# Kernel optimization log

Measured on AMD Instinct MI355X. Metric: run time of the kernel, lower is better.

Reference implementation:

```python
import jax, jax.numpy as jnp
import numpy as np


def binarize(x):
    # sign to +/-1 (>=0 -> 1); forward value only (STE handled in bwd module)
    return jnp.where(x >= 0, 1.0, -1.0).astype(x.dtype)


def setup_inputs() -> dict:
    key = jax.random.key(0)
    k1, k2, k3 = jax.random.split(key, 3)
    B, D_IN, D_H, D_OUT = 16384, 4096, 4096, 1
    x = jax.random.normal(k1, (B, D_IN), dtype=jnp.float32)
    W1 = jax.random.normal(k2, (D_H, D_IN), dtype=jnp.float32) * 0.02
    W2 = jax.random.normal(k3, (D_OUT, D_H), dtype=jnp.float32) * 0.02
    return {"x": x, "W1": W1, "W2": W2}


def reference(x, W1, W2):
    # fc1: BinaryLinear (binarized weight, no bias) + BinaryTanh (hardtanh then sign)
    h = x @ binarize(W1).T                      # [B, D_H]
    h = binarize(jnp.clip(h, -1.0, 1.0))        # hardtanh + binarize -> +/-1
    # fc2: BinaryLinear + Sigmoid
    out = jax.nn.sigmoid(h @ binarize(W2).T)    # [B, 1]
    y_hat = jnp.squeeze((out >= 0.5).astype(jnp.float32))  # [B]
    return out, y_hat
```

## Files before the change

kernel.cpp:

```cpp
#include <hip/hip_runtime.h>
#include <stdint.h>


typedef int v4i  __attribute__((ext_vector_type(4)));
typedef int v16i __attribute__((ext_vector_type(16)));

#define B_ROWS   16384
#define DIM      4096
#define MT       64
#define NT       128
#define KT       64

#define WS_LOGIT  0
#define WS_W2S    65536
#define WS_B      69632
#define WS_A      (69632 + 16777216)
#define WS_NEEDED ((size_t)WS_A + 268435456ULL)

__device__ __forceinline__ void dma16(const void* g, void* l) {
    __builtin_amdgcn_global_load_lds(
        (const __attribute__((address_space(1))) void*)g,
        (__attribute__((address_space(3))) void*)l, 16, 0, 0);
}

__global__ void pack_x_frag_kernel(const float* __restrict__ x, int8_t* __restrict__ wsA) {
    __shared__ __align__(16) int8_t tile[16384];
    const int mb32 = blockIdx.x, t = threadIdx.x;
    const int r = t >> 3;
    const int c = t & 7;
    const int kh = (c >> 2) & 1;
    const int L = kh * 32 + r;
    const int ldsQ = L * 16 + (c & 3) * 4;
    const float* srcRow = x + ((size_t)(mb32 * 32 + r) << 12);
    int8_t* dstBase = wsA + ((size_t)mb32 << 19);

    for (int kw = 0; kw < 32; ++kw) {
#pragma unroll
        for (int i = 0; i < 4; ++i) {
            const int j = c + 8 * i;
            float4 f = ((const float4*)(srcRow + (kw << 7)))[j];
            float fv[4] = {f.x, f.y, f.z, f.w};
            int dig[4][4];
#pragma unroll
            for (int e = 0; e < 4; ++e) {
                int v = __float2int_rn(fv[e] * 67108864.0f);
#pragma unroll
                for (int d = 0; d < 4; ++d) {
                    int b = (int)(int8_t)(v & 0xff);
                    dig[e][d] = b & 0xff;
                    v = (v - b) >> 8;
                }
            }
#pragma unroll
            for (int d = 0; d < 4; ++d) {
                uint32_t wrd = (uint32_t)dig[0][d] | ((uint32_t)dig[1][d] << 8)
                             | ((uint32_t)dig[2][d] << 16) | ((uint32_t)dig[3][d] << 24);
                *(uint32_t*)(tile + i * 4096 + d * 1024 + ldsQ) = wrd;
            }
        }
        __syncthreads();
        {
            const int4* s = (const int4*)tile;
            int4* dst = (int4*)(dstBase + ((size_t)kw << 14));
#pragma unroll
            for (int q = 0; q < 4; ++q) dst[t + 256 * q] = s[t + 256 * q];
        }
        __syncthreads();
    }
}

__global__ void pack_x_kernel(float* __restrict__ x) {
    const int b = blockIdx.x, t = threadIdx.x;
    float* row = x + (size_t)b * DIM;
    float f[16];
#pragma unroll
    for (int i = 0; i < 4; ++i) {
        float4 v = ((const float4*)(row + t * 16))[i];
        f[i*4+0] = v.x; f[i*4+1] = v.y; f[i*4+2] = v.z; f[i*4+3] = v.w;
    }
    __syncthreads();
    uint32_t wds[4][4];
#pragma unroll
    for (int j = 0; j < 4; ++j) {
#pragma unroll
        for (int d = 0; d < 4; ++d) wds[d][j] = 0u;
#pragma unroll
        for (int i = 0; i < 4; ++i) {
            int v = __float2int_rn(f[j*4+i] * 67108864.0f);
#pragma unroll
            for (int d = 0; d < 4; ++d) {
                int bb = (int)(int8_t)(v & 0xff);
                wds[d][j] |= (uint32_t)(bb & 0xff) << (8 * i);
                v = (v - bb) >> 8;
            }
        }
    }
    int8_t* rowb = (int8_t*)row;
#pragma unroll
    for (int d = 0; d < 4; ++d) {
        int4 o; o.x = (int)wds[d][0]; o.y = (int)wds[d][1];
        o.z = (int)wds[d][2]; o.w = (int)wds[d][3];
        *(int4*)(rowb + d * DIM + t * 16) = o;
    }
}

__global__ void pack_w1_kernel(const float* __restrict__ W1, int8_t* __restrict__ wsB) {
    const int tg = blockIdx.x * 256 + threadIdx.x;
    const int n  = tg >> 8;
    const int k0 = (tg & 255) << 4;
    const float* src = W1 + (size_t)n * DIM + k0;
    uint32_t w[4];
#pragma unroll
    for (int j = 0; j < 4; ++j) {
        float4 v = ((const float4*)src)[j];
        uint32_t b0 = (v.x >= 0.f) ? 0x01u : 0xFFu;
        uint32_t b1 = (v.y >= 0.f) ? 0x01u : 0xFFu;
        uint32_t b2 = (v.z >= 0.f) ? 0x01u : 0xFFu;
        uint32_t b3 = (v.w >= 0.f) ? 0x01u : 0xFFu;
        w[j] = b0 | (b1 << 8) | (b2 << 16) | (b3 << 24);
    }
    const int nb = n >> 7, kt = k0 >> 6;
    const int nsub = (n >> 5) & 3, ks = (k0 >> 5) & 1;
    const int L = (n & 31) | (((k0 >> 4) & 1) << 5);
    const size_t off = ((size_t)(nb * 64 + kt) << 13) + (nsub << 11) + (ks << 10) + (L << 4);
    int4 o; o.x = (int)w[0]; o.y = (int)w[1]; o.z = (int)w[2]; o.w = (int)w[3];
    *(int4*)(wsB + off) = o;
}

__global__ void pack_w2_kernel(const float* __restrict__ W2, int8_t* __restrict__ w2s) {
    const int j = blockIdx.x * 256 + threadIdx.x;
    if (j < DIM) w2s[j] = (W2[j] >= 0.f) ? (int8_t)1 : (int8_t)-1;
}

#define LOAD_AF(dst, kt_) do {                                             \
    const int8_t* _p = aBase + ((size_t)(kt_) << 13);                      \
    _Pragma("unroll") for (int _s = 0; _s < 2; ++_s)                       \
    _Pragma("unroll") for (int _d = 0; _d < 4; ++_d)                       \
        dst[_s * 4 + _d] = *(const v4i*)(_p + (_s << 12) + (_d << 10));    \
} while (0)

#define DMA_B(kt_, buf_) do {                                              \
    const int8_t* _s = bSrcL + ((size_t)(kt_) << 13);                      \
    int8_t* _dst = &bT[(buf_)][w << 11];                                   \
    dma16(_s, _dst); dma16(_s + 1024, _dst + 1024);                        \
} while (0)

#define MFMA_STEP(af_, buf_) do {                                          \
    const int8_t* _bc = &bT[(buf_)][(wx << 12) + (lane << 4)];             \
    v4i _bf[2][2];                                                         \
    _Pragma("unroll") for (int _s = 0; _s < 2; ++_s)                       \
    _Pragma("unroll") for (int _n = 0; _n < 2; ++_n)                       \
        _bf[_s][_n] = *(const v4i*)(_bc + (_n << 11) + (_s << 10));        \
    _Pragma("unroll") for (int _s = 0; _s < 2; ++_s)                       \
    _Pragma("unroll") for (int _n = 0; _n < 2; ++_n)                       \
    _Pragma("unroll") for (int _d = 0; _d < 4; ++_d)                       \
        acc[_n][_d] = __builtin_amdgcn_mfma_i32_32x32x32_i8(               \
            af_[_s * 4 + _d], _bf[_s][_n], acc[_n][_d], 0, 0, 0);          \
} while (0)

__launch_bounds__(256, 2)
__global__ void gemm_direct_kernel(const int8_t* __restrict__ wsA,
                                   const int8_t* __restrict__ wsB,
                                   const int8_t* __restrict__ w2s,
                                   int* __restrict__ logit) {
    __shared__ __align__(16) int8_t bT[2][8192];

    const int bid = blockIdx.x;
    const int nb = bid & 31, mb = bid >> 5;
    const int t = threadIdx.x, lane = t & 63, w = t >> 6;
    const int wy = w >> 1, wx = w & 1;

    v16i acc[2][4];
#pragma unroll
    for (int n = 0; n < 2; ++n)
#pragma unroll
        for (int d = 0; d < 4; ++d)
#pragma unroll
            for (int i = 0; i < 16; ++i) acc[n][d][i] = 0;

    const int8_t* aBase = wsA + ((size_t)(mb * 2 + wy) << 19) + (lane << 4);
    const int8_t* bSrcL = wsB + ((size_t)(nb * 64) << 13) + (w << 11) + (lane << 4);

    v4i afA[8], afB[8];
    DMA_B(0, 0);
    LOAD_AF(afA, 0);

    for (int kt2 = 0; kt2 < 32; ++kt2) {
        const int kt = kt2 * 2;
        __syncthreads();
        if (kt < 63) { DMA_B(kt + 1, 1); LOAD_AF(afB, kt + 1); }
        MFMA_STEP(afA, 0);
        __syncthreads();
        if (kt2 < 31) { DMA_B(kt + 2, 0); LOAD_AF(afA, kt + 2); }
        MFMA_STEP(afB, 1);
    }

    const int half = lane >> 5, col = lane & 31;
    int psum[16];
#pragma unroll
    for (int r = 0; r < 16; ++r) psum[r] = 0;
#pragma unroll
    for (int n = 0; n < 2; ++n) {
        const int j = nb * NT + wx * 64 + n * 32 + col;
        const int w2v = (int)w2s[j];
#pragma unroll
        for (int r = 0; r < 16; ++r) {
            long long h = (long long)acc[n][0][r]
                        + ((long long)acc[n][1][r] << 8)
                        + ((long long)acc[n][2][r] << 16)
                        + ((long long)acc[n][3][r] << 24);
            psum[r] += (h >= 0) ? w2v : -w2v;
        }
    }
#pragma unroll
    for (int r = 0; r < 16; ++r) {
#pragma unroll
        for (int m = 1; m <= 16; m <<= 1)
            psum[r] += __shfl_xor(psum[r], m, 64);
    }
    if (col == 0) {
        const int rowBase = mb * MT + wy * 32 + 4 * half;
#pragma unroll
        for (int r = 0; r < 16; ++r)
            atomicAdd(logit + rowBase + (r & 3) + 8 * (r >> 2), psum[r]);
    }
}

__launch_bounds__(256, 2)
__global__ void gemm_kernel(const int8_t* __restrict__ xq,
                            const int8_t* __restrict__ wsB,
                            const int8_t* __restrict__ w2s,
                            int* __restrict__ logit) {
    __shared__ __align__(16) int8_t aT[4 * MT * KT];
    __shared__ __align__(16) int8_t bT[NT * KT];

    const int bid = blockIdx.x;
    const int nb = bid & 31, mb = bid >> 5;
    const int t = threadIdx.x, lane = t & 63, w = t >> 6;
    const int wy = w >> 1, wx = w & 1;

    v16i acc[2][4];
#pragma unroll
    for (int n = 0; n < 2; ++n)
#pragma unroll
        for (int d = 0; d < 4; ++d)
#pragma unroll
            for (int i = 0; i < 16; ++i) acc[n][d][i] = 0;

    const int8_t* aSrc = xq + (size_t)(mb * MT + lane) * (4 * DIM) + w * DIM;
    const int8_t* bSrc = wsB + ((size_t)(nb * 64) << 13) + t * 32;
    const int aDst = w * (MT * KT) + ((lane >> 5) << 11) + ((lane & 31) << 4);

    for (int kt = 0; kt < DIM / KT; ++kt) {
#pragma unroll
        for (int k16 = 0; k16 < 4; ++k16) {
            v4i v = *(const v4i*)(aSrc + kt * KT + k16 * 16);
            *(v4i*)(aT + aDst + ((k16 >> 1) << 10) + ((k16 & 1) << 9)) = v;
        }
        {
            const v4i* s = (const v4i*)(bSrc + ((size_t)kt << 13));
            *(v4i*)(bT + t * 32)      = s[0];
            *(v4i*)(bT + t * 32 + 16) = s[1];
        }
        __syncthreads();
#pragma unroll
        for (int s = 0; s < 2; ++s) {
            v4i af[4], bf[2];
#pragma unroll
            for (int d = 0; d < 4; ++d)
                af[d] = *(const v4i*)(aT + d * (MT * KT) + (wy << 11) + (s << 10) + (lane << 4));
#pragma unroll
            for (int n = 0; n < 2; ++n)
                bf[n] = *(const v4i*)(bT + ((wx * 2 + n) << 11) + (s << 10) + (lane << 4));
#pragma unroll
            for (int n = 0; n < 2; ++n)
#pragma unroll
                for (int d = 0; d < 4; ++d)
                    acc[n][d] = __builtin_amdgcn_mfma_i32_32x32x32_i8(af[d], bf[n], acc[n][d], 0, 0, 0);
        }
        __syncthreads();
    }

    const int half = lane >> 5, col = lane & 31;
    int psum[16];
#pragma unroll
    for (int r = 0; r < 16; ++r) psum[r] = 0;
#pragma unroll
    for (int n = 0; n < 2; ++n) {
        const int j = nb * NT + wx * 64 + n * 32 + col;
        const int w2v = (int)w2s[j];
#pragma unroll
        for (int r = 0; r < 16; ++r) {
            long long h = (long long)acc[n][0][r]
                        + ((long long)acc[n][1][r] << 8)
                        + ((long long)acc[n][2][r] << 16)
                        + ((long long)acc[n][3][r] << 24);
            psum[r] += (h >= 0) ? w2v : -w2v;
        }
    }
#pragma unroll
    for (int r = 0; r < 16; ++r) {
#pragma unroll
        for (int m = 1; m <= 16; m <<= 1)
            psum[r] += __shfl_xor(psum[r], m, 64);
    }
    if (col == 0) {
        const int rowBase = mb * MT + wy * 32 + 4 * half;
#pragma unroll
        for (int r = 0; r < 16; ++r)
            atomicAdd(logit + rowBase + (r & 3) + 8 * (r >> 2), psum[r]);
    }
}

__global__ void finalize_kernel(const int* __restrict__ logit, float* __restrict__ out) {
    const int b = blockIdx.x * 256 + threadIdx.x;
    if (b < B_ROWS) {
        const int l = logit[b];
        out[b]          = 1.f / (1.f + expf(-(float)l));
        out[B_ROWS + b] = (l >= 0) ? 1.f : 0.f;
    }
}

extern "C" void kernel_launch(void* const* d_in, const int* in_sizes, int n_in,
                              void* d_out, int out_size, void* d_ws, size_t ws_size,
                              hipStream_t stream) {
    float*       x   = (float*)d_in[0];
    const float* W1  = (const float*)d_in[1];
    const float* W2  = (const float*)d_in[2];
    float*       out = (float*)d_out;

    int8_t* ws    = (int8_t*)d_ws;
    int*    logit = (int*)(ws + WS_LOGIT);
    int8_t* w2s   = ws + WS_W2S;
    int8_t* wsB   = ws + WS_B;

    hipMemsetAsync(logit, 0, B_ROWS * sizeof(int), stream);
    pack_w1_kernel<<<DIM, 256, 0, stream>>>(W1, wsB);
    pack_w2_kernel<<<16, 256, 0, stream>>>(W2, w2s);

    if (ws_size >= WS_NEEDED) {
        int8_t* wsA = ws + WS_A;
        pack_x_frag_kernel<<<B_ROWS / 32, 256, 0, stream>>>(x, wsA);
        gemm_direct_kernel<<<(B_ROWS / MT) * (DIM / NT), 256, 0, stream>>>(wsA, wsB, w2s, logit);
    } else {
        pack_x_kernel<<<B_ROWS, 256, 0, stream>>>(x);
        gemm_kernel<<<(B_ROWS / MT) * (DIM / NT), 256, 0, stream>>>((const int8_t*)x, wsB, w2s, logit);
    }
    finalize_kernel<<<B_ROWS / 256, 256, 0, stream>>>(logit, out);
}
```

Before: 1.671 ms.

## Stage A and B tiles through LDS with a triple-buffered async DMA pipeline

A fragments were previously loaded directly from global memory into registers and B was double-buffered in LDS. Now both A and B tiles are DMA'd into a three-stage LDS ring with global_load_lds, issued two steps ahead. Each step waits with explicit vmcnt/lgkmcnt counters and one barrier instead of two syncthreads. This aims to hide global latency better and free registers, at the cost of three times 24KB of LDS per block, which may limit occupancy, plus the extra LDS reads for A.

```diff
diff --git a/kernel.cpp b/kernel.cpp
--- a/kernel.cpp
+++ b/kernel.cpp
@@ -132,30 +132,49 @@
     if (j < DIM) w2s[j] = (W2[j] >= 0.f) ? (int8_t)1 : (int8_t)-1;
 }
 
-#define LOAD_AF(dst, kt_) do {                                             \
-    const int8_t* _p = aBase + ((size_t)(kt_) << 13);                      \
-    _Pragma("unroll") for (int _s = 0; _s < 2; ++_s)                       \
-    _Pragma("unroll") for (int _d = 0; _d < 4; ++_d)                       \
-        dst[_s * 4 + _d] = *(const v4i*)(_p + (_s << 12) + (_d << 10));    \
+#define STGB 24576
+
+#define PIPE_BARRIER(N) do {                                               \
+    __builtin_amdgcn_sched_barrier(0);                                     \
+    asm volatile("s_waitcnt vmcnt(" #N ") lgkmcnt(0)" ::: "memory");       \
+    __builtin_amdgcn_s_barrier();                                          \
+    __builtin_amdgcn_sched_barrier(0);                                     \
 } while (0)
 
-#define DMA_B(kt_, buf_) do {                                              \
-    const int8_t* _s = bSrcL + ((size_t)(kt_) << 13);                      \
-    int8_t* _dst = &bT[(buf_)][w << 11];                                   \
-    dma16(_s, _dst); dma16(_s + 1024, _dst + 1024);                        \
+#define ISSUE_STAGE(kt_, ib) do {                                          \
+    const int8_t* _ga = gA + ((size_t)(kt_) << 13);                        \
+    const int8_t* _gb = gB + ((size_t)(kt_) << 13);                        \
+    int8_t* _ad = &stg[ib][w << 12];                                       \
+    int8_t* _bd = &stg[ib][16384 + (w << 11)];                             \
+    dma16(_ga,        _ad);                                                \
+    dma16(_ga + 1024, _ad + 1024);                                         \
+    dma16(_ga + 2048, _ad + 2048);                                         \
+    dma16(_ga + 3072, _ad + 3072);                                         \
+    dma16(_gb,        _bd);                                                \
+    dma16(_gb + 1024, _bd + 1024);                                         \
 } while (0)
 
-#define MFMA_STEP(af_, buf_) do {                                          \
-    const int8_t* _bc = &bT[(buf_)][(wx << 12) + (lane << 4)];             \
-    v4i _bf[2][2];                                                         \
-    _Pragma("unroll") for (int _s = 0; _s < 2; ++_s)                       \
-    _Pragma("unroll") for (int _n = 0; _n < 2; ++_n)                       \
-        _bf[_s][_n] = *(const v4i*)(_bc + (_n << 11) + (_s << 10));        \
+#define MFMA_STAGE(cb) do {                                                \
+    const int8_t* _ab = &stg[cb][(wy << 13) + (lane << 4)];                \
+    const int8_t* _bb = &stg[cb][16384 + (wx << 12) + (lane << 4)];        \
+    v4i _af[2][4], _bf[2][2];                                              \
+    _Pragma("unroll") for (int _s = 0; _s < 2; ++_s) {                     \
+        _Pragma("unroll") for (int _d = 0; _d < 4; ++_d)                   \
+            _af[_s][_d] = *(const v4i*)(_ab + (_s << 12) + (_d << 10));    \
+        _Pragma("unroll") for (int _n = 0; _n < 2; ++_n)                   \
+            _bf[_s][_n] = *(const v4i*)(_bb + (_n << 11) + (_s << 10));    \
+    }                                                                      \
     _Pragma("unroll") for (int _s = 0; _s < 2; ++_s)                       \
     _Pragma("unroll") for (int _n = 0; _n < 2; ++_n)                       \
     _Pragma("unroll") for (int _d = 0; _d < 4; ++_d)                       \
         acc[_n][_d] = __builtin_amdgcn_mfma_i32_32x32x32_i8(               \
-            af_[_s * 4 + _d], _bf[_s][_n], acc[_n][_d], 0, 0, 0);          \
+            _af[_s][_d], _bf[_s][_n], acc[_n][_d], 0, 0, 0);               \
+} while (0)
+
+#define STEP(kt_, cb, ib) do {                                             \
+    PIPE_BARRIER(6);                                                       \
+    ISSUE_STAGE((kt_) + 2, ib);                                            \
+    MFMA_STAGE(cb);                                                        \
 } while (0)
 
 __launch_bounds__(256, 2)
@@ -163,7 +182,7 @@
                                    const int8_t* __restrict__ wsB,
                                    const int8_t* __restrict__ w2s,
                                    int* __restrict__ logit) {
-    __shared__ __align__(16) int8_t bT[2][8192];
+    __shared__ __align__(16) int8_t stg[3][STGB];
 
     const int bid = blockIdx.x;
     const int nb = bid & 31, mb = bid >> 5;
@@ -178,22 +197,24 @@
 #pragma unroll
             for (int i = 0; i < 16; ++i) acc[n][d][i] = 0;
 
-    const int8_t* aBase = wsA + ((size_t)(mb * 2 + wy) << 19) + (lane << 4);
-    const int8_t* bSrcL = wsB + ((size_t)(nb * 64) << 13) + (w << 11) + (lane << 4);
-
-    v4i afA[8], afB[8];
-    DMA_B(0, 0);
-    LOAD_AF(afA, 0);
-
-    for (int kt2 = 0; kt2 < 32; ++kt2) {
-        const int kt = kt2 * 2;
-        __syncthreads();
-        if (kt < 63) { DMA_B(kt + 1, 1); LOAD_AF(afB, kt + 1); }
-        MFMA_STEP(afA, 0);
-        __syncthreads();
-        if (kt2 < 31) { DMA_B(kt + 2, 0); LOAD_AF(afA, kt + 2); }
-        MFMA_STEP(afB, 1);
-    }
+    const int8_t* gA = wsA + ((size_t)(mb * 2 + (w >> 1)) << 19) + ((w & 1) << 12) + (lane << 4);
+    const int8_t* gB = wsB + ((size_t)(nb * 64) << 13) + (w << 11) + (lane << 4);
+
+    ISSUE_STAGE(0, 0);
+    ISSUE_STAGE(1, 1);
+
+#pragma unroll 1
+    for (int kt = 0; kt < 60; kt += 3) {
+        STEP(kt,     0, 2);
+        STEP(kt + 1, 1, 0);
+        STEP(kt + 2, 2, 1);
+    }
+    STEP(60, 0, 2);
+    STEP(61, 1, 0);
+    PIPE_BARRIER(6);
+    MFMA_STAGE(2);
+    PIPE_BARRIER(0);
+    MFMA_STAGE(0);
 
     const int half = lane >> 5, col = lane & 31;
     int psum[16];
```

New measurement: 1.443 ms. 1.16x faster.

## Triple-buffer B tiles in LDS with single barrier and explicit vmcnt waits

Applied to the files above, without the earlier changes.

Replaces the double-buffered B staging, which used two __syncthreads per pair of k-steps, with a three-stage LDS ring. Each k-step now has one barrier with a partial s_waitcnt vmcnt(2), so the B DMA for k+2 stays in flight while the MFMAs for k run. The loop is unrolled by 6 so buffer indices are compile-time constants, and sched_barriers pin the issue order. This costs an extra 8 KB of LDS per block, and correctness now depends on the hand-counted vmcnt values matching the real number of outstanding loads.

```diff
diff --git a/kernel.cpp b/kernel.cpp
--- a/kernel.cpp
+++ b/kernel.cpp
@@ -132,25 +132,34 @@
     if (j < DIM) w2s[j] = (W2[j] >= 0.f) ? (int8_t)1 : (int8_t)-1;
 }
 
+#define STGB 8192
+
+#define PIPE_BARRIER(N) do {                                               \
+    __builtin_amdgcn_sched_barrier(0);                                     \
+    asm volatile("s_waitcnt vmcnt(" #N ") lgkmcnt(0)" ::: "memory");       \
+    __builtin_amdgcn_s_barrier();                                          \
+    __builtin_amdgcn_sched_barrier(0);                                     \
+} while (0)
+
 #define LOAD_AF(dst, kt_) do {                                             \
-    const int8_t* _p = aBase + ((size_t)(kt_) << 13);                      \
+    const int8_t* _p = gA + ((size_t)(kt_) << 13);                         \
     _Pragma("unroll") for (int _s = 0; _s < 2; ++_s)                       \
     _Pragma("unroll") for (int _d = 0; _d < 4; ++_d)                       \
         dst[_s * 4 + _d] = *(const v4i*)(_p + (_s << 12) + (_d << 10));    \
 } while (0)
 
-#define DMA_B(kt_, buf_) do {                                              \
-    const int8_t* _s = bSrcL + ((size_t)(kt_) << 13);                      \
-    int8_t* _dst = &bT[(buf_)][w << 11];                                   \
+#define DMA_B(kt_, ib) do {                                                \
+    const int8_t* _s = gB + ((size_t)(kt_) << 13);                         \
+    int8_t* _dst = &stg[ib][w << 11];                                      \
     dma16(_s, _dst); dma16(_s + 1024, _dst + 1024);                        \
 } while (0)
 
-#define MFMA_STEP(af_, buf_) do {                                          \
-    const int8_t* _bc = &bT[(buf_)][(wx << 12) + (lane << 4)];             \
+#define MFMA_STAGE(af_, cb) do {                                           \
+    const int8_t* _bb = &stg[cb][(wx << 12) + (lane << 4)];                \
     v4i _bf[2][2];                                                         \
     _Pragma("unroll") for (int _s = 0; _s < 2; ++_s)                       \
     _Pragma("unroll") for (int _n = 0; _n < 2; ++_n)                       \
-        _bf[_s][_n] = *(const v4i*)(_bc + (_n << 11) + (_s << 10));        \
+        _bf[_s][_n] = *(const v4i*)(_bb + (_n << 11) + (_s << 10));        \
     _Pragma("unroll") for (int _s = 0; _s < 2; ++_s)                       \
     _Pragma("unroll") for (int _n = 0; _n < 2; ++_n)                       \
     _Pragma("unroll") for (int _d = 0; _d < 4; ++_d)                       \
@@ -158,12 +167,20 @@
             af_[_s * 4 + _d], _bf[_s][_n], acc[_n][_d], 0, 0, 0);          \
 } while (0)
 
+#define STEP(kt_, ca_reg, cb, ia_reg, ib) do {                             \
+    PIPE_BARRIER(2);                                                       \
+    LOAD_AF(ia_reg, (kt_) + 1);                                            \
+    DMA_B((kt_) + 2, ib);                                                  \
+    __builtin_amdgcn_sched_barrier(0);                                     \
+    MFMA_STAGE(ca_reg, cb);                                                \
+} while (0)
+
 __launch_bounds__(256, 2)
 __global__ void gemm_direct_kernel(const int8_t* __restrict__ wsA,
                                    const int8_t* __restrict__ wsB,
                                    const int8_t* __restrict__ w2s,
                                    int* __restrict__ logit) {
-    __shared__ __align__(16) int8_t bT[2][8192];
+    __shared__ __align__(16) int8_t stg[3][STGB];
 
     const int bid = blockIdx.x;
     const int nb = bid & 31, mb = bid >> 5;
@@ -178,22 +195,31 @@
 #pragma unroll
             for (int i = 0; i < 16; ++i) acc[n][d][i] = 0;
 
-    const int8_t* aBase = wsA + ((size_t)(mb * 2 + wy) << 19) + (lane << 4);
-    const int8_t* bSrcL = wsB + ((size_t)(nb * 64) << 13) + (w << 11) + (lane << 4);
+    const int8_t* gA = wsA + ((size_t)(mb * 2 + wy) << 19) + (lane << 4);
+    const int8_t* gB = wsB + ((size_t)(nb * 64) << 13) + (w << 11) + (lane << 4);
 
     v4i afA[8], afB[8];
     DMA_B(0, 0);
     LOAD_AF(afA, 0);
-
-    for (int kt2 = 0; kt2 < 32; ++kt2) {
-        const int kt = kt2 * 2;
-        __syncthreads();
-        if (kt < 63) { DMA_B(kt + 1, 1); LOAD_AF(afB, kt + 1); }
-        MFMA_STEP(afA, 0);
-        __syncthreads();
-        if (kt2 < 31) { DMA_B(kt + 2, 0); LOAD_AF(afA, kt + 2); }
-        MFMA_STEP(afB, 1);
-    }
+    DMA_B(1, 1);
+
+#pragma unroll 1
+    for (int kt = 0; kt < 60; kt += 6) {
+        STEP(kt + 0, afA, 0, afB, 2);
+        STEP(kt + 1, afB, 1, afA, 0);
+        STEP(kt + 2, afA, 2, afB, 1);
+        STEP(kt + 3, afB, 0, afA, 2);
+        STEP(kt + 4, afA, 1, afB, 0);
+        STEP(kt + 5, afB, 2, afA, 1);
+    }
+    STEP(60, afA, 0, afB, 2);
+    STEP(61, afB, 1, afA, 0);
+    PIPE_BARRIER(2);
+    LOAD_AF(afB, 63);
+    __builtin_amdgcn_sched_barrier(0);
+    MFMA_STAGE(afA, 2);
+    PIPE_BARRIER(0);
+    MFMA_STAGE(afB, 0);
 
     const int half = lane >> 5, col = lane & 31;
     int psum[16];
```

Result: no change. 1.687 ms (+0.9%).

## Stage A tiles through LDS with a three-stage pipeline and keep B in registers

Applied to the files above, without the earlier changes.

Swaps which operand goes through shared memory. A tiles (shared by the two wx waves) are now DMA'd into a three-buffer LDS ring, while B fragments load straight into registers two steps ahead. Explicit waitcnt, barriers and sched_barriers set the overlap, and setprio raises wave priority during the MFMA burst. This aims to hide global latency better and halve redundant A global reads. The cost is more LDS (48KB per block), which may limit occupancy at two blocks per CU, plus fragile hand-tuned vmcnt counts.

```diff
diff --git a/kernel.cpp b/kernel.cpp
--- a/kernel.cpp
+++ b/kernel.cpp
@@ -132,30 +132,52 @@
     if (j < DIM) w2s[j] = (W2[j] >= 0.f) ? (int8_t)1 : (int8_t)-1;
 }
 
-#define LOAD_AF(dst, kt_) do {                                             \
-    const int8_t* _p = aBase + ((size_t)(kt_) << 13);                      \
+#define STGB 16384
+
+#define PIPE_BARRIER(N) do {                                               \
+    __builtin_amdgcn_sched_barrier(0);                                     \
+    asm volatile("s_waitcnt vmcnt(" #N ") lgkmcnt(0)" ::: "memory");       \
+    __builtin_amdgcn_s_barrier();                                          \
+    __builtin_amdgcn_sched_barrier(0);                                     \
+} while (0)
+
+#define LOAD_BF(dst, kt_) do {                                             \
+    const int8_t* _p = gBr + ((size_t)(kt_) << 13);                        \
+    _Pragma("unroll") for (int _s = 0; _s < 2; ++_s)                       \
+    _Pragma("unroll") for (int _n = 0; _n < 2; ++_n)                       \
+        dst[_s][_n] = *(const v4i*)(_p + (_n << 11) + (_s << 10));         \
+} while (0)
+
+#define DMA_A(kt_, ib) do {                                                \
+    const int8_t* _s = gA + ((size_t)(kt_) << 13);                         \
+    int8_t* _dst = &stg[ib][w << 12];                                      \
+    dma16(_s,        _dst);                                                \
+    dma16(_s + 1024, _dst + 1024);                                         \
+    dma16(_s + 2048, _dst + 2048);                                         \
+    dma16(_s + 3072, _dst + 3072);                                         \
+} while (0)
+
+#define MFMA_STAGE(cb, bf_) do {                                           \
+    const int8_t* _ab = &stg[cb][(wy << 13) + (lane << 4)];                \
+    v4i _af[2][4];                                                         \
     _Pragma("unroll") for (int _s = 0; _s < 2; ++_s)                       \
     _Pragma("unroll") for (int _d = 0; _d < 4; ++_d)                       \
-        dst[_s * 4 + _d] = *(const v4i*)(_p + (_s << 12) + (_d << 10));    \
-} while (0)
-
-#define DMA_B(kt_, buf_) do {                                              \
-    const int8_t* _s = bSrcL + ((size_t)(kt_) << 13);                      \
-    int8_t* _dst = &bT[(buf_)][w << 11];                                   \
-    dma16(_s, _dst); dma16(_s + 1024, _dst + 1024);                        \
-} while (0)
-
-#define MFMA_STEP(af_, buf_) do {                                          \
-    const int8_t* _bc = &bT[(buf_)][(wx << 12) + (lane << 4)];             \
-    v4i _bf[2][2];                                                         \
-    _Pragma("unroll") for (int _s = 0; _s < 2; ++_s)                       \
-    _Pragma("unroll") for (int _n = 0; _n < 2; ++_n)                       \
-        _bf[_s][_n] = *(const v4i*)(_bc + (_n << 11) + (_s << 10));        \
+        _af[_s][_d] = *(const v4i*)(_ab + (_s << 12) + (_d << 10));        \
+    __builtin_amdgcn_s_setprio(1);                                         \
     _Pragma("unroll") for (int _s = 0; _s < 2; ++_s)                       \
     _Pragma("unroll") for (int _n = 0; _n < 2; ++_n)                       \
     _Pragma("unroll") for (int _d = 0; _d < 4; ++_d)                       \
         acc[_n][_d] = __builtin_amdgcn_mfma_i32_32x32x32_i8(               \
-            af_[_s * 4 + _d], _bf[_s][_n], acc[_n][_d], 0, 0, 0);          \
+            _af[_s][_d], bf_[_s][_n], acc[_n][_d], 0, 0, 0);               \
+    __builtin_amdgcn_s_setprio(0);                                         \
+} while (0)
+
+#define STEP(kt_, cb, bfc, bfi, ib) do {                                   \
+    PIPE_BARRIER(8);                                                       \
+    LOAD_BF(bfi, (kt_) + 2);                                               \
+    DMA_A((kt_) + 2, ib);                                                  \
+    __builtin_amdgcn_sched_barrier(0);                                     \
+    MFMA_STAGE(cb, bfc);                                                   \
 } while (0)
 
 __launch_bounds__(256, 2)
@@ -163,7 +185,7 @@
                                    const int8_t* __restrict__ wsB,
                                    const int8_t* __restrict__ w2s,
                                    int* __restrict__ logit) {
-    __shared__ __align__(16) int8_t bT[2][8192];
+    __shared__ __align__(16) int8_t stg[3][STGB];
 
     const int bid = blockIdx.x;
     const int nb = bid & 31, mb = bid >> 5;
@@ -178,22 +200,27 @@
 #pragma unroll
             for (int i = 0; i < 16; ++i) acc[n][d][i] = 0;
 
-    const int8_t* aBase = wsA + ((size_t)(mb * 2 + wy) << 19) + (lane << 4);
-    const int8_t* bSrcL = wsB + ((size_t)(nb * 64) << 13) + (w << 11) + (lane << 4);
-
-    v4i afA[8], afB[8];
-    DMA_B(0, 0);
-    LOAD_AF(afA, 0);
-
-    for (int kt2 = 0; kt2 < 32; ++kt2) {
-        const int kt = kt2 * 2;
-        __syncthreads();
-        if (kt < 63) { DMA_B(kt + 1, 1); LOAD_AF(afB, kt + 1); }
-        MFMA_STEP(afA, 0);
-        __syncthreads();
-        if (kt2 < 31) { DMA_B(kt + 2, 0); LOAD_AF(afA, kt + 2); }
-        MFMA_STEP(afB, 1);
-    }
+    const int8_t* gA  = wsA + ((size_t)(mb * 2 + wy) << 19) + ((size_t)wx << 12) + (lane << 4);
+    const int8_t* gBr = wsB + ((size_t)(nb * 64) << 13) + ((size_t)wx << 12) + (lane << 4);
+
+    v4i bf0[2][2], bf1[2][2], bf2[2][2];
+    LOAD_BF(bf0, 0);
+    DMA_A(0, 0);
+    LOAD_BF(bf1, 1);
+    DMA_A(1, 1);
+
+#pragma unroll 1
+    for (int kt = 0; kt < 60; kt += 3) {
+        STEP(kt + 0, 0, bf0, bf2, 2);
+        STEP(kt + 1, 1, bf1, bf0, 0);
+        STEP(kt + 2, 2, bf2, bf1, 1);
+    }
+    STEP(60, 0, bf0, bf2, 2);
+    STEP(61, 1, bf1, bf0, 0);
+    PIPE_BARRIER(8);
+    MFMA_STAGE(2, bf2);
+    PIPE_BARRIER(0);
+    MFMA_STAGE(0, bf0);
 
     const int half = lane >> 5, col = lane & 31;
     int psum[16];
```

After: 1.554 ms. 1.08x faster.
